# Optimization experiments

Measured on AMD Instinct MI355X. Metric: run time of the kernel, lower is better.

The kernel has to match this reference:

```python
import jax, jax.numpy as jnp
import numpy as np

B, T, D, H = 4, 2048, 1024, 16
HS = D // H  # 64
EPS = 1e-5


def layer_norm(x, g, b):
    mu = jnp.mean(x, axis=-1, keepdims=True)
    var = jnp.mean(jnp.square(x - mu), axis=-1, keepdims=True)
    return (x - mu) * jax.lax.rsqrt(var + EPS) * g + b


def setup_inputs() -> dict:
    key = jax.random.key(0)
    ks = jax.random.split(key, 12)
    s_in = 1.0 / np.sqrt(D)
    s_proj = 1.0 / np.sqrt(H * HS)
    s_ff = 1.0 / np.sqrt(4 * D)
    return {
        "x": jax.random.normal(ks[0], (B, T, D), jnp.float32),
        "ln1_g": jnp.ones((D,), jnp.float32),
        "ln1_b": jnp.zeros((D,), jnp.float32),
        # per-head Q/K/V weights stacked: [H, D, HS] (x @ W, no bias)
        "wq": jax.random.uniform(ks[1], (H, D, HS), jnp.float32, -s_in, s_in),
        "wk": jax.random.uniform(ks[2], (H, D, HS), jnp.float32, -s_in, s_in),
        "wv": jax.random.uniform(ks[3], (H, D, HS), jnp.float32, -s_in, s_in),
        "w_proj": jax.random.uniform(ks[4], (H * HS, D), jnp.float32, -s_proj, s_proj),
        "b_proj": jax.random.uniform(ks[5], (D,), jnp.float32, -s_proj, s_proj),
        "ln2_g": jnp.ones((D,), jnp.float32),
        "ln2_b": jnp.zeros((D,), jnp.float32),
        "w1": jax.random.uniform(ks[6], (D, 4 * D), jnp.float32, -s_in, s_in),
        "b1": jax.random.uniform(ks[7], (4 * D,), jnp.float32, -s_in, s_in),
        "w2": jax.random.uniform(ks[8], (4 * D, D), jnp.float32, -s_ff, s_ff),
        "b2": jax.random.uniform(ks[9], (D,), jnp.float32, -s_ff, s_ff),
    }


def reference(x, ln1_g, ln1_b, wq, wk, wv, w_proj, b_proj, ln2_g, ln2_b, w1, b1, w2, b2):
    # --- pre-LN self-attention ---
    xn = layer_norm(x, ln1_g, ln1_b)
    q = jnp.einsum("btd,hdk->bhtk", xn, wq)
    k = jnp.einsum("btd,hdk->bhtk", xn, wk)
    v = jnp.einsum("btd,hdk->bhtk", xn, wv)
    scale = HS ** -0.5
    scores = jnp.einsum("bhtk,bhsk->bhts", q, k) * scale  # [B,H,T,T]
    t = x.shape[1]
    causal = jnp.tril(jnp.ones((t, t), bool))
    scores = jnp.where(causal, scores, -jnp.inf)
    attn = jax.nn.softmax(scores, axis=-1)  # dropout p=0 -> identity
    ctx = jnp.einsum("bhts,bhsk->bhtk", attn, v)
    ctx = jnp.transpose(ctx, (0, 2, 1, 3)).reshape(x.shape[0], t, H * HS)
    x = x + ctx @ w_proj + b_proj
    # --- pre-LN feed-forward ---
    xn = layer_norm(x, ln2_g, ln2_b)
    h = jax.nn.relu(xn @ w1 + b1)
    return x + h @ w2 + b2
```

## Files before the change

### kernel.cpp

```cpp
#include <hip/hip_runtime.h>

typedef __bf16 bf16;
typedef __attribute__((ext_vector_type(8))) __bf16 bf16x8;
typedef __attribute__((ext_vector_type(4))) __bf16 bf16x4;
typedef __attribute__((ext_vector_type(4))) float f32x4;

static constexpr int Bc = 4, Tc = 2048, Dc = 1024, Hc = 16, HSc = 64, DFF = 4096;
static constexpr int Mrows = Bc * Tc;

#define DEV __device__ __forceinline__

DEV void load_lds16(const void* g, void* l) {
  __builtin_amdgcn_global_load_lds(
      (const __attribute__((address_space(1))) void*)g,
      (__attribute__((address_space(3))) void*)l, 16, 0, 0);
}

__global__ void repack_qkv_kernel(const float* __restrict__ wq,
                                  const float* __restrict__ wk,
                                  const float* __restrict__ wv,
                                  bf16* __restrict__ dst) {
  __shared__ float tile[64][65];
  const int dblk = blockIdx.x;
  const int z = blockIdx.y;
  const int w = z >> 4, h = z & 15;
  const float* src = (w == 0 ? wq : (w == 1 ? wk : wv)) + (size_t)h * Dc * HSc;
  const int tx = threadIdx.x, ty = threadIdx.y;
#pragma unroll
  for (int i = 0; i < 16; ++i)
    tile[ty + i * 4][tx] = src[(size_t)(dblk * 64 + ty + i * 4) * HSc + tx];
  __syncthreads();
#pragma unroll
  for (int i = 0; i < 16; ++i) {
    const int s = ty + i * 4;
    dst[((size_t)w * 1024 + h * 64 + s) * Dc + dblk * 64 + tx] = (bf16)tile[tx][s];
  }
}

__global__ void transpose_to_bf16_kernel(const float* __restrict__ src,
                                         bf16* __restrict__ dst, int R, int C) {
  __shared__ float tile[64][65];
  const int r0 = blockIdx.x * 64, c0 = blockIdx.y * 64;
  const int tx = threadIdx.x, ty = threadIdx.y;
#pragma unroll
  for (int i = 0; i < 16; ++i)
    tile[ty + i * 4][tx] = src[(size_t)(r0 + ty + i * 4) * C + c0 + tx];
  __syncthreads();
#pragma unroll
  for (int i = 0; i < 16; ++i)
    dst[(size_t)(c0 + ty + i * 4) * R + r0 + tx] = (bf16)tile[tx][ty + i * 4];
}

__global__ __launch_bounds__(256) void ln_kernel(const float* __restrict__ x,
                                                 const float* __restrict__ gam,
                                                 const float* __restrict__ bet,
                                                 bf16* __restrict__ out) {
  const int row = blockIdx.x;
  const int t = threadIdx.x;
  const float4 v = ((const float4*)(x + (size_t)row * Dc))[t];
  float s = v.x + v.y + v.z + v.w;
  float s2 = v.x * v.x + v.y * v.y + v.z * v.z + v.w * v.w;
#pragma unroll
  for (int m = 1; m < 64; m <<= 1) {
    s += __shfl_xor(s, m);
    s2 += __shfl_xor(s2, m);
  }
  __shared__ float red[8];
  const int wid = t >> 6;
  if ((t & 63) == 0) { red[wid * 2] = s; red[wid * 2 + 1] = s2; }
  __syncthreads();
  s = red[0] + red[2] + red[4] + red[6];
  s2 = red[1] + red[3] + red[5] + red[7];
  const float mean = s * (1.f / Dc);
  const float var = s2 * (1.f / Dc) - mean * mean;
  const float rstd = rsqrtf(var + 1e-5f);
  const float4 gv = ((const float4*)gam)[t];
  const float4 bv = ((const float4*)bet)[t];
  bf16x4 o;
  o[0] = (bf16)((v.x - mean) * rstd * gv.x + bv.x);
  o[1] = (bf16)((v.y - mean) * rstd * gv.y + bv.y);
  o[2] = (bf16)((v.z - mean) * rstd * gv.z + bv.z);
  o[3] = (bf16)((v.w - mean) * rstd * gv.w + bv.w);
  *(bf16x4*)(out + (size_t)row * Dc + t * 4) = o;
}

template <int MODE, int KTOT, int BN>
__global__ __launch_bounds__(512, 1) void gemm4p_kernel(
    const bf16* __restrict__ A, const bf16* __restrict__ BT,
    const float* __restrict__ bias, const float* __restrict__ resid,
    float* __restrict__ outf, bf16* __restrict__ outb,
    bf16* __restrict__ qo, bf16* __restrict__ ko, bf16* __restrict__ vto) {
  constexpr int NT = KTOT / 32;
  constexpr int L = (BN == 256) ? 4 : 3;
  constexpr int WN = (BN == 256) ? 4 : 2;
  constexpr int MW = (BN == 256) ? 128 : 64;
  constexpr int NAF = MW / 16;
  constexpr int NSTR = (MODE == 2) ? 4096 : 1024;
  constexpr int ABUF = 256 * 32 * 2;
  constexpr int BBUF = BN * 32 * 2;

  __shared__ __attribute__((aligned(16))) bf16 As[4][256 * 32];
  __shared__ __attribute__((aligned(16))) bf16 Bs[4][BN * 32];

  const int tid = threadIdx.x;
  const int wid = tid >> 6, lane = tid & 63;
  const int g = (lane >> 4) & 3, c = lane & 15;
  const int wm = wid / WN, wn = wid % WN;
  const int bm = blockIdx.x, bn = blockIdx.y;

  f32x4 acc[NAF][4];
#pragma unroll
  for (int i = 0; i < NAF; ++i)
#pragma unroll
    for (int j = 0; j < 4; ++j)
#pragma unroll
      for (int r = 0; r < 4; ++r) acc[i][j][r] = 0.f;

  const int sof = ((tid & 3) ^ ((tid >> 3) & 3)) << 4;
  const char* Agl = (const char*)A;
  const char* Bgl = (const char*)BT;

  auto stage = [&](int kt) {
    const int buf = kt & 3;
    const size_t kb = (size_t)kt * 64;
#pragma unroll
    for (int a = 0; a < 2; ++a)
      load_lds16(Agl + ((size_t)(bm * 256 + a * 128 + (tid >> 2)) * KTOT) * 2 + kb + sof,
                 (char*)&As[buf][0] + a * 8192 + tid * 16);
    if (BN == 256) {
#pragma unroll
      for (int a = 0; a < 2; ++a)
        load_lds16(Bgl + ((size_t)(bn * 256 + a * 128 + (tid >> 2)) * KTOT) * 2 + kb + sof,
                   (char*)&Bs[buf][0] + a * 8192 + tid * 16);
    } else {
      load_lds16(Bgl + ((size_t)(bn * 128 + (tid >> 2)) * KTOT) * 2 + kb + sof,
                 (char*)&Bs[buf][0] + tid * 16);
    }
  };

  stage(0);
  stage(1);
  stage(2);

  for (int t = 0; t < NT; ++t) {
    if (t + 2 < NT) {
      asm volatile("s_waitcnt vmcnt(%0)" ::"i"(2 * L) : "memory");
    } else if (t + 1 < NT) {
      asm volatile("s_waitcnt vmcnt(%0)" ::"i"(L) : "memory");
    } else {
      asm volatile("s_waitcnt vmcnt(0)" ::: "memory");
    }
    __builtin_amdgcn_s_barrier();
    if (t + 3 < NT) stage(t + 3);

    const char* Ab = (const char*)As + (t & 3) * ABUF;
    const char* Bb = (const char*)Bs + (t & 3) * BBUF;
    bf16x8 bfr[4], af[NAF];
#pragma unroll
    for (int j = 0; j < 4; ++j) {
      const int row = wn * 64 + j * 16 + c;
      bfr[j] = *(const bf16x8*)(Bb + row * 64 + ((g * 16) ^ (((row >> 1) & 3) << 4)));
    }
#pragma unroll
    for (int i = 0; i < NAF; ++i) {
      const int row = wm * MW + i * 16 + c;
      af[i] = *(const bf16x8*)(Ab + row * 64 + ((g * 16) ^ (((row >> 1) & 3) << 4)));
    }
    if (NAF == 8) {
      asm volatile("s_waitcnt lgkmcnt(4)" ::: "memory");
    } else {
      asm volatile("s_waitcnt lgkmcnt(0)" ::: "memory");
    }
    __builtin_amdgcn_sched_barrier(0);
    __builtin_amdgcn_s_setprio(1);
#pragma unroll
    for (int i = 0; i < 4; ++i)
#pragma unroll
      for (int j = 0; j < 4; ++j)
        acc[i][j] = __builtin_amdgcn_mfma_f32_16x16x32_bf16(af[i], bfr[j], acc[i][j], 0, 0, 0);
    __builtin_amdgcn_s_setprio(0);
    if (NAF == 8) {
      asm volatile("s_waitcnt lgkmcnt(0)" ::: "memory");
      __builtin_amdgcn_sched_barrier(0);
      __builtin_amdgcn_s_setprio(1);
#pragma unroll
      for (int i = 4; i < NAF; ++i)
#pragma unroll
        for (int j = 0; j < 4; ++j)
          acc[i][j] = __builtin_amdgcn_mfma_f32_16x16x32_bf16(af[i], bfr[j], acc[i][j], 0, 0, 0);
      __builtin_amdgcn_s_setprio(0);
    }
  }

#pragma unroll
  for (int nf = 0; nf < 4; ++nf) {
    const int n = bn * BN + wn * 64 + nf * 16 + c;
    float bi = 0.f;
    if (MODE != 0) bi = bias[n];
#pragma unroll
    for (int fr = 0; fr < NAF; ++fr) {
      const int m0 = bm * 256 + wm * MW + fr * 16 + g * 4;
      if (MODE == 0) {
        const int w = n >> 10, n1 = n & 1023, h = n1 >> 6, sidx = n1 & 63;
        const int b2 = m0 >> 11, t0 = m0 & 2047;
        if (w == 0) {
#pragma unroll
          for (int r = 0; r < 4; ++r)
            qo[(size_t)(b2 * Hc + h) * (Tc * HSc) + (size_t)(t0 + r) * HSc + sidx] =
                (bf16)(acc[fr][nf][r] * 0.125f);
        } else if (w == 1) {
#pragma unroll
          for (int r = 0; r < 4; ++r)
            ko[(size_t)(b2 * Hc + h) * (Tc * HSc) + (size_t)(t0 + r) * HSc + sidx] =
                (bf16)acc[fr][nf][r];
        } else {
          bf16x4 pk;
#pragma unroll
          for (int r = 0; r < 4; ++r) pk[r] = (bf16)acc[fr][nf][r];
          *(bf16x4*)&vto[((size_t)(b2 * Hc + h) * HSc + sidx) * Tc + t0] = pk;
        }
      } else if (MODE == 1 || MODE == 3) {
#pragma unroll
        for (int r = 0; r < 4; ++r) {
          const size_t idx = (size_t)(m0 + r) * NSTR + n;
          outf[idx] = acc[fr][nf][r] + bi + resid[idx];
        }
      } else {
#pragma unroll
        for (int r = 0; r < 4; ++r)
          outb[(size_t)(m0 + r) * NSTR + n] = (bf16)fmaxf(acc[fr][nf][r] + bi, 0.f);
      }
    }
  }
}

__global__ __launch_bounds__(256, 2) void attn_kernel(const bf16* __restrict__ q,
                                                      const bf16* __restrict__ k,
                                                      const bf16* __restrict__ vt,
                                                      bf16* __restrict__ ctx) {
  __shared__ __attribute__((aligned(16))) bf16 Kl[2][4096];
  __shared__ __attribute__((aligned(16))) bf16 Vl[2][4096];
  __shared__ __attribute__((aligned(16))) bf16 P[4][32][72];
  const int d0 = blockIdx.x;
  const int L = (d0 & 7) * 64 + (d0 >> 3);
  const int bh = L >> 3, p = L & 7;
  const int tid = threadIdx.x;
  const int wid = tid >> 6, lane = tid & 63;
  const int g = lane >> 4, c = lane & 15;
  const bf16* qh = q + (size_t)bh * Tc * HSc;
  const char* kh = (const char*)(k + (size_t)bh * Tc * HSc);
  const char* vh = (const char*)(vt + (size_t)bh * HSc * Tc);
  const int b = bh >> 4, h = bh & 15;

  const int sw = ((lane >> 3) & 7) << 4;
  const int soK = (lane * 16) ^ sw;
  const int vrow = lane >> 3;
  const int vcol = ((lane & 7) * 16) ^ sw;
  const int rsw = (c & 7) << 4;

  for (int g2 = 0; g2 < 2; ++g2) {
    const int grp = g2 ? p : 15 - p;
    const int ktB = 2 * grp + 1;
    const int ktW = 2 * grp + (wid >> 1);
    const int row0 = grp * 128 + wid * 32;
    const bf16* qb = qh + (size_t)row0 * HSc;

    bf16x8 qf[2][2];
#pragma unroll
    for (int mi = 0; mi < 2; ++mi)
#pragma unroll
      for (int kk = 0; kk < 2; ++kk)
        qf[mi][kk] = *(const bf16x8*)&qb[(size_t)(mi * 16 + c) * HSc + kk * 32 + g * 8];

    f32x4 o[2][4];
    float m_[2][4], ls[2][4];
#pragma unroll
    for (int mi = 0; mi < 2; ++mi)
#pragma unroll
      for (int r = 0; r < 4; ++r) {
        m_[mi][r] = -1e30f;
        ls[mi][r] = 0.f;
#pragma unroll
        for (int di = 0; di < 4; ++di) o[mi][di][r] = 0.f;
      }

    auto stage = [&](int buf, int kt) {
      const char* kb = kh + (size_t)kt * 8192;
      const char* vb = vh + (size_t)kt * 128;
#pragma unroll
      for (int i = 0; i < 4; ++i) {
        const int idx = wid * 4 + i;
        if (idx < 8) {
          load_lds16(kb + idx * 1024 + soK, (char*)&Kl[buf][0] + idx * 1024);
        } else {
          const int j = idx - 8;
          load_lds16(vb + (size_t)(j * 8 + vrow) * (Tc * 2) + vcol,
                     (char*)&Vl[buf][0] + j * 1024);
        }
      }
    };

    stage(0, 0);
    __syncthreads();
    int cur = 0;
    for (int kt = 0; kt <= ktB; ++kt) {
      if (kt < ktB) stage(cur ^ 1, kt + 1);
      if (kt <= ktW) {
        const char* Kb = (const char*)&Kl[cur][0];
        bf16x8 kf[4][2];
#pragma unroll
        for (int ni = 0; ni < 4; ++ni)
#pragma unroll
          for (int kk = 0; kk < 2; ++kk)
            kf[ni][kk] = *(const bf16x8*)(Kb + (ni * 16 + c) * 128 +
                                          (((kk << 6) | (g << 4)) ^ rsw));
        f32x4 s[2][4];
#pragma unroll
        for (int mi = 0; mi < 2; ++mi)
#pragma unroll
          for (int ni = 0; ni < 4; ++ni)
#pragma unroll
            for (int r = 0; r < 4; ++r) s[mi][ni][r] = 0.f;
        __builtin_amdgcn_s_setprio(1);
#pragma unroll
        for (int kk = 0; kk < 2; ++kk)
#pragma unroll
          for (int mi = 0; mi < 2; ++mi)
#pragma unroll
            for (int ni = 0; ni < 4; ++ni)
              s[mi][ni] = __builtin_amdgcn_mfma_f32_16x16x32_bf16(qf[mi][kk], kf[ni][kk],
                                                                  s[mi][ni], 0, 0, 0);
        __builtin_amdgcn_s_setprio(0);

        if (kt == ktW) {
#pragma unroll
          for (int mi = 0; mi < 2; ++mi)
#pragma unroll
            for (int ni = 0; ni < 4; ++ni)
#pragma unroll
              for (int r = 0; r < 4; ++r) {
                const int row = row0 + mi * 16 + g * 4 + r;
                const int col = kt * 64 + ni * 16 + c;
                if (col > row) s[mi][ni][r] = -1e30f;
              }
        }

        float pm[2][4];
        int need = 0;
#pragma unroll
        for (int mi = 0; mi < 2; ++mi)
#pragma unroll
          for (int r = 0; r < 4; ++r) {
            pm[mi][r] =
                fmaxf(fmaxf(s[mi][0][r], s[mi][1][r]), fmaxf(s[mi][2][r], s[mi][3][r]));
            need |= (pm[mi][r] > m_[mi][r] + 8.f) ? 1 : 0;
          }
        if (__any(need)) {
#pragma unroll
          for (int mi = 0; mi < 2; ++mi)
#pragma unroll
            for (int r = 0; r < 4; ++r) {
              float mx = pm[mi][r];
#pragma unroll
              for (int msk = 1; msk < 16; msk <<= 1) mx = fmaxf(mx, __shfl_xor(mx, msk));
              const float mn = fmaxf(m_[mi][r], mx);
              const float al = __expf(m_[mi][r] - mn);
              m_[mi][r] = mn;
              ls[mi][r] *= al;
#pragma unroll
              for (int di = 0; di < 4; ++di) o[mi][di][r] *= al;
            }
        }
#pragma unroll
        for (int mi = 0; mi < 2; ++mi)
#pragma unroll
          for (int r = 0; r < 4; ++r) {
            float ps = 0.f;
#pragma unroll
            for (int ni = 0; ni < 4; ++ni) {
              const float pv = __expf(s[mi][ni][r] - m_[mi][r]);
              ps += pv;
              P[wid][mi * 16 + g * 4 + r][ni * 16 + c] = (bf16)pv;
            }
            ls[mi][r] += ps;
          }
        asm volatile("s_waitcnt lgkmcnt(0)" ::: "memory");
        __builtin_amdgcn_sched_barrier(0);

        bf16x8 pf[2][2];
#pragma unroll
        for (int mi = 0; mi < 2; ++mi)
#pragma unroll
          for (int kk = 0; kk < 2; ++kk)
            pf[mi][kk] = *(const bf16x8*)&P[wid][mi * 16 + c][kk * 32 + g * 8];
        const char* Vb = (const char*)&Vl[cur][0];
#pragma unroll
        for (int di = 0; di < 4; ++di) {
          bf16x8 vf0 = *(const bf16x8*)(Vb + (di * 16 + c) * 128 + ((g << 4) ^ rsw));
          bf16x8 vf1 =
              *(const bf16x8*)(Vb + (di * 16 + c) * 128 + (((1 << 6) | (g << 4)) ^ rsw));
          __builtin_amdgcn_s_setprio(1);
#pragma unroll
          for (int mi = 0; mi < 2; ++mi) {
            o[mi][di] = __builtin_amdgcn_mfma_f32_16x16x32_bf16(pf[mi][0], vf0, o[mi][di], 0, 0, 0);
            o[mi][di] = __builtin_amdgcn_mfma_f32_16x16x32_bf16(pf[mi][1], vf1, o[mi][di], 0, 0, 0);
          }
          __builtin_amdgcn_s_setprio(0);
        }
      }
      __syncthreads();
      cur ^= 1;
    }

#pragma unroll
    for (int mi = 0; mi < 2; ++mi)
#pragma unroll
      for (int r = 0; r < 4; ++r) {
        float l = ls[mi][r];
#pragma unroll
        for (int msk = 1; msk < 16; msk <<= 1) l += __shfl_xor(l, msk);
        const float inv = 1.f / l;
        const int t = row0 + mi * 16 + g * 4 + r;
#pragma unroll
        for (int di = 0; di < 4; ++di)
          ctx[((size_t)(b * Tc + t)) * Dc + h * 64 + di * 16 + c] =
              (bf16)(o[mi][di][r] * inv);
      }
  }
}

extern "C" void kernel_launch(void* const* d_in, const int* in_sizes, int n_in,
                              void* d_out, int out_size, void* d_ws, size_t ws_size,
                              hipStream_t stream) {
  (void)in_sizes; (void)n_in; (void)out_size; (void)ws_size;
  const float* x      = (const float*)d_in[0];
  const float* ln1_g  = (const float*)d_in[1];
  const float* ln1_b  = (const float*)d_in[2];
  const float* wq     = (const float*)d_in[3];
  const float* wk     = (const float*)d_in[4];
  const float* wv     = (const float*)d_in[5];
  const float* w_proj = (const float*)d_in[6];
  const float* b_proj = (const float*)d_in[7];
  const float* ln2_g  = (const float*)d_in[8];
  const float* ln2_b  = (const float*)d_in[9];
  const float* w1     = (const float*)d_in[10];
  const float* b1     = (const float*)d_in[11];
  const float* w2     = (const float*)d_in[12];
  const float* b2     = (const float*)d_in[13];
  float* out = (float*)d_out;
  char* ws = (char*)d_ws;

  bf16* qbuf   = (bf16*)(ws + 0);
  bf16* kbuf   = (bf16*)(ws + 16777216);
  bf16* vtbuf  = (bf16*)(ws + 33554432);
  bf16* ctxbuf = (bf16*)(ws + 50331648);
  bf16* wqkvT  = (bf16*)(ws + 67108864);
  bf16* hbuf   = (bf16*)(ws + 0);
  bf16* wprojT = (bf16*)(ws + 73400320);
  bf16* w1T    = (bf16*)(ws + 75497472);
  bf16* w2T    = (bf16*)(ws + 83886080);
  bf16* xn     = (bf16*)(ws + 92274688);
  float* x1buf = (float*)(ws + 109051904);

  repack_qkv_kernel<<<dim3(16, 48), dim3(64, 4), 0, stream>>>(wq, wk, wv, wqkvT);
  transpose_to_bf16_kernel<<<dim3(16, 16), dim3(64, 4), 0, stream>>>(w_proj, wprojT, 1024, 1024);
  transpose_to_bf16_kernel<<<dim3(16, 64), dim3(64, 4), 0, stream>>>(w1, w1T, 1024, 4096);
  transpose_to_bf16_kernel<<<dim3(64, 16), dim3(64, 4), 0, stream>>>(w2, w2T, 4096, 1024);

  ln_kernel<<<Mrows, 256, 0, stream>>>(x, ln1_g, ln1_b, xn);
  gemm4p_kernel<0, 1024, 256><<<dim3(32, 12), 512, 0, stream>>>(
      xn, wqkvT, nullptr, nullptr, nullptr, nullptr, qbuf, kbuf, vtbuf);
  attn_kernel<<<512, 256, 0, stream>>>(qbuf, kbuf, vtbuf, ctxbuf);
  gemm4p_kernel<1, 1024, 128><<<dim3(32, 8), 512, 0, stream>>>(
      ctxbuf, wprojT, b_proj, x, x1buf, nullptr, nullptr, nullptr, nullptr);
  ln_kernel<<<Mrows, 256, 0, stream>>>(x1buf, ln2_g, ln2_b, xn);
  gemm4p_kernel<2, 1024, 256><<<dim3(32, 16), 512, 0, stream>>>(
      xn, w1T, b1, nullptr, nullptr, hbuf, nullptr, nullptr, nullptr);
  gemm4p_kernel<3, 4096, 128><<<dim3(32, 8), 512, 0, stream>>>(
      hbuf, w2T, b2, x1buf, out, nullptr, nullptr, nullptr, nullptr);
}
```

Baseline: 437.8 us.

## Restructure GEMM into 8-phase ping-pong pipeline with 64-wide K steps

Replaces the 4-buffer, 32-wide-K GEMM pipeline with a two-sided double buffer over 64-wide K tiles, split into two 32-wide halves. Global-to-LDS staging for future tiles is interleaved between MFMA phases, with barriers separating the phases, so memory traffic overlaps compute more finely. Warp tiling changes (4x2 warps for the BN=128 path), and the QKV projection now uses BN=128 tiles on a wider grid. The XOR swizzle on LDS reads is removed, which may introduce bank conflicts, and the extra barriers add synchronisation cost.

Result: faster. 385.1 us (-12.0%).

```diff
diff --git a/kernel.cpp b/kernel.cpp
--- a/kernel.cpp
+++ b/kernel.cpp
@@ -85,27 +85,26 @@
 }
 
 template <int MODE, int KTOT, int BN>
-__global__ __launch_bounds__(512, 1) void gemm4p_kernel(
+__global__ __launch_bounds__(512, 1) void gemm8p_kernel(
     const bf16* __restrict__ A, const bf16* __restrict__ BT,
     const float* __restrict__ bias, const float* __restrict__ resid,
     float* __restrict__ outf, bf16* __restrict__ outb,
     bf16* __restrict__ qo, bf16* __restrict__ ko, bf16* __restrict__ vto) {
-  constexpr int NT = KTOT / 32;
-  constexpr int L = (BN == 256) ? 4 : 3;
-  constexpr int WN = (BN == 256) ? 4 : 2;
-  constexpr int MW = (BN == 256) ? 128 : 64;
+  constexpr int NT = KTOT / 64;
+  constexpr int NSTR = (MODE == 2) ? 4096 : 1024;
+  constexpr int WMD = (BN == 256) ? 2 : 4;
+  constexpr int MW = 256 / WMD;
   constexpr int NAF = MW / 16;
-  constexpr int NSTR = (MODE == 2) ? 4096 : 1024;
-  constexpr int ABUF = 256 * 32 * 2;
-  constexpr int BBUF = BN * 32 * 2;
-
-  __shared__ __attribute__((aligned(16))) bf16 As[4][256 * 32];
-  __shared__ __attribute__((aligned(16))) bf16 Bs[4][BN * 32];
+  constexpr int NBI = BN / 128;
+
+  __shared__ __attribute__((aligned(16))) bf16 As[2][2][256 * 32];
+  __shared__ __attribute__((aligned(16))) bf16 Bs[2][2][BN * 32];
 
   const int tid = threadIdx.x;
   const int wid = tid >> 6, lane = tid & 63;
   const int g = (lane >> 4) & 3, c = lane & 15;
-  const int wm = wid / WN, wn = wid % WN;
+  const int wmi = (BN == 256) ? (wid >> 2) : (wid >> 1);
+  const int wni = (BN == 256) ? (wid & 3) : (wid & 1);
   const int bm = blockIdx.x, bn = blockIdx.y;
 
   f32x4 acc[NAF][4];
@@ -116,90 +115,165 @@
 #pragma unroll
       for (int r = 0; r < 4; ++r) acc[i][j][r] = 0.f;
 
-  const int sof = ((tid & 3) ^ ((tid >> 3) & 3)) << 4;
   const char* Agl = (const char*)A;
   const char* Bgl = (const char*)BT;
-
-  auto stage = [&](int kt) {
-    const int buf = kt & 3;
-    const size_t kb = (size_t)kt * 64;
+  const int grow = tid >> 2;
+  const int gcol = (tid & 3) * 8;
+
+  auto stageA = [&](int side, int ks, int kt) {
 #pragma unroll
     for (int a = 0; a < 2; ++a)
-      load_lds16(Agl + ((size_t)(bm * 256 + a * 128 + (tid >> 2)) * KTOT) * 2 + kb + sof,
-                 (char*)&As[buf][0] + a * 8192 + tid * 16);
+      load_lds16(
+          Agl + ((size_t)(bm * 256 + a * 128 + grow) * KTOT + kt * 64 + ks * 32 + gcol) * 2,
+          (char*)&As[side][ks][0] + a * 8192 + tid * 16);
+  };
+  auto stageB = [&](int side, int ks, int kt) {
+#pragma unroll
+    for (int b = 0; b < NBI; ++b)
+      load_lds16(
+          Bgl + ((size_t)(bn * BN + b * 128 + grow) * KTOT + kt * 64 + ks * 32 + gcol) * 2,
+          (char*)&Bs[side][ks][0] + b * 8192 + tid * 16);
+  };
+
+  const int aoff = (wmi * MW + c) * 64 + g * 16;
+  const int boff = (wni * 64 + c) * 64 + g * 16;
+
+  if (BN == 256) {
+    stageB(0, 0, 0); stageA(0, 0, 0); stageB(0, 1, 0); stageA(0, 1, 0);
+    stageB(1, 0, 1); stageA(1, 0, 1); stageB(1, 1, 1);
+    asm volatile("s_waitcnt vmcnt(6)" ::: "memory");
+  } else {
+    stageA(0, 0, 0); stageB(0, 0, 0); stageA(0, 1, 0); stageB(0, 1, 0);
+    stageA(1, 0, 1); stageB(1, 0, 1);
+    asm volatile("s_waitcnt vmcnt(3)" ::: "memory");
+  }
+  __builtin_amdgcn_s_barrier();
+
+  for (int t = 0; t < NT; ++t) {
+    const int s = t & 1, ns = s ^ 1;
+    const char* Ab0 = (const char*)&As[s][0][0] + aoff;
+    const char* Ab1 = (const char*)&As[s][1][0] + aoff;
+    const char* Bb0 = (const char*)&Bs[s][0][0] + boff;
+    const char* Bb1 = (const char*)&Bs[s][1][0] + boff;
+    bf16x8 af[4], bfr[4];
+
     if (BN == 256) {
 #pragma unroll
-      for (int a = 0; a < 2; ++a)
-        load_lds16(Bgl + ((size_t)(bn * 256 + a * 128 + (tid >> 2)) * KTOT) * 2 + kb + sof,
-                   (char*)&Bs[buf][0] + a * 8192 + tid * 16);
-    } else {
-      load_lds16(Bgl + ((size_t)(bn * 128 + (tid >> 2)) * KTOT) * 2 + kb + sof,
-                 (char*)&Bs[buf][0] + tid * 16);
-    }
-  };
-
-  stage(0);
-  stage(1);
-  stage(2);
-
-  for (int t = 0; t < NT; ++t) {
-    if (t + 2 < NT) {
-      asm volatile("s_waitcnt vmcnt(%0)" ::"i"(2 * L) : "memory");
-    } else if (t + 1 < NT) {
-      asm volatile("s_waitcnt vmcnt(%0)" ::"i"(L) : "memory");
-    } else {
-      asm volatile("s_waitcnt vmcnt(0)" ::: "memory");
-    }
-    __builtin_amdgcn_s_barrier();
-    if (t + 3 < NT) stage(t + 3);
-
-    const char* Ab = (const char*)As + (t & 3) * ABUF;
-    const char* Bb = (const char*)Bs + (t & 3) * BBUF;
-    bf16x8 bfr[4], af[NAF];
-#pragma unroll
-    for (int j = 0; j < 4; ++j) {
-      const int row = wn * 64 + j * 16 + c;
-      bfr[j] = *(const bf16x8*)(Bb + row * 64 + ((g * 16) ^ (((row >> 1) & 3) << 4)));
-    }
-#pragma unroll
-    for (int i = 0; i < NAF; ++i) {
-      const int row = wm * MW + i * 16 + c;
-      af[i] = *(const bf16x8*)(Ab + row * 64 + ((g * 16) ^ (((row >> 1) & 3) << 4)));
-    }
-    if (NAF == 8) {
-      asm volatile("s_waitcnt lgkmcnt(4)" ::: "memory");
-    } else {
-      asm volatile("s_waitcnt lgkmcnt(0)" ::: "memory");
-    }
-    __builtin_amdgcn_sched_barrier(0);
-    __builtin_amdgcn_s_setprio(1);
-#pragma unroll
-    for (int i = 0; i < 4; ++i)
-#pragma unroll
-      for (int j = 0; j < 4; ++j)
-        acc[i][j] = __builtin_amdgcn_mfma_f32_16x16x32_bf16(af[i], bfr[j], acc[i][j], 0, 0, 0);
-    __builtin_amdgcn_s_setprio(0);
-    if (NAF == 8) {
+      for (int f = 0; f < 4; ++f) af[f] = *(const bf16x8*)(Ab0 + f * 1024);
+#pragma unroll
+      for (int j = 0; j < 4; ++j) bfr[j] = *(const bf16x8*)(Bb0 + j * 1024);
+      if (t + 1 < NT) stageA(ns, 1, t + 1);
+      __builtin_amdgcn_s_barrier();
       asm volatile("s_waitcnt lgkmcnt(0)" ::: "memory");
       __builtin_amdgcn_sched_barrier(0);
       __builtin_amdgcn_s_setprio(1);
 #pragma unroll
-      for (int i = 4; i < NAF; ++i)
+      for (int f = 0; f < 4; ++f)
 #pragma unroll
         for (int j = 0; j < 4; ++j)
-          acc[i][j] = __builtin_amdgcn_mfma_f32_16x16x32_bf16(af[i], bfr[j], acc[i][j], 0, 0, 0);
+          acc[f][j] = __builtin_amdgcn_mfma_f32_16x16x32_bf16(af[f], bfr[j], acc[f][j], 0, 0, 0);
       __builtin_amdgcn_s_setprio(0);
+      __builtin_amdgcn_s_barrier();
+#pragma unroll
+      for (int f = 0; f < 4; ++f) af[f] = *(const bf16x8*)(Ab0 + (4 + f) * 1024);
+      if (t + 2 < NT) stageB(s, 0, t + 2);
+      __builtin_amdgcn_s_barrier();
+      asm volatile("s_waitcnt lgkmcnt(0)" ::: "memory");
+      __builtin_amdgcn_sched_barrier(0);
+      __builtin_amdgcn_s_setprio(1);
+#pragma unroll
+      for (int f = 0; f < 4; ++f)
+#pragma unroll
+        for (int j = 0; j < 4; ++j)
+          acc[4 + f][j] =
+              __builtin_amdgcn_mfma_f32_16x16x32_bf16(af[f], bfr[j], acc[4 + f][j], 0, 0, 0);
+      __builtin_amdgcn_s_setprio(0);
+      __builtin_amdgcn_s_barrier();
+#pragma unroll
+      for (int f = 0; f < 4; ++f) af[f] = *(const bf16x8*)(Ab1 + f * 1024);
+#pragma unroll
+      for (int j = 0; j < 4; ++j) bfr[j] = *(const bf16x8*)(Bb1 + j * 1024);
+      if (t + 2 < NT) stageA(s, 0, t + 2);
+      __builtin_amdgcn_s_barrier();
+      asm volatile("s_waitcnt lgkmcnt(0)" ::: "memory");
+      __builtin_amdgcn_sched_barrier(0);
+      __builtin_amdgcn_s_setprio(1);
+#pragma unroll
+      for (int f = 0; f < 4; ++f)
+#pragma unroll
+        for (int j = 0; j < 4; ++j)
+          acc[f][j] = __builtin_amdgcn_mfma_f32_16x16x32_bf16(af[f], bfr[j], acc[f][j], 0, 0, 0);
+      __builtin_amdgcn_s_setprio(0);
+      __builtin_amdgcn_s_barrier();
+#pragma unroll
+      for (int f = 0; f < 4; ++f) af[f] = *(const bf16x8*)(Ab1 + (4 + f) * 1024);
+      if (t + 2 < NT) stageB(s, 1, t + 2);
+      __builtin_amdgcn_s_barrier();
+      asm volatile("s_waitcnt lgkmcnt(0)" ::: "memory");
+      __builtin_amdgcn_sched_barrier(0);
+      __builtin_amdgcn_s_setprio(1);
+#pragma unroll
+      for (int f = 0; f < 4; ++f)
+#pragma unroll
+        for (int j = 0; j < 4; ++j)
+          acc[4 + f][j] =
+              __builtin_amdgcn_mfma_f32_16x16x32_bf16(af[f], bfr[j], acc[4 + f][j], 0, 0, 0);
+      __builtin_amdgcn_s_setprio(0);
+      if (t + 2 < NT) {
+        asm volatile("s_waitcnt vmcnt(6)" ::: "memory");
+      } else {
+        asm volatile("s_waitcnt vmcnt(0)" ::: "memory");
+      }
+      __builtin_amdgcn_s_barrier();
+    } else {
+#pragma unroll
+      for (int f = 0; f < 4; ++f) af[f] = *(const bf16x8*)(Ab0 + f * 1024);
+#pragma unroll
+      for (int j = 0; j < 4; ++j) bfr[j] = *(const bf16x8*)(Bb0 + j * 1024);
+      if (t + 1 < NT) { stageA(ns, 1, t + 1); stageB(ns, 1, t + 1); }
+      __builtin_amdgcn_s_barrier();
+      asm volatile("s_waitcnt lgkmcnt(0)" ::: "memory");
+      __builtin_amdgcn_sched_barrier(0);
+      __builtin_amdgcn_s_setprio(1);
+#pragma unroll
+      for (int f = 0; f < 4; ++f)
+#pragma unroll
+        for (int j = 0; j < 4; ++j)
+          acc[f][j] = __builtin_amdgcn_mfma_f32_16x16x32_bf16(af[f], bfr[j], acc[f][j], 0, 0, 0);
+      __builtin_amdgcn_s_setprio(0);
+      __builtin_amdgcn_s_barrier();
+#pragma unroll
+      for (int f = 0; f < 4; ++f) af[f] = *(const bf16x8*)(Ab1 + f * 1024);
+#pragma unroll
+      for (int j = 0; j < 4; ++j) bfr[j] = *(const bf16x8*)(Bb1 + j * 1024);
+      if (t + 2 < NT) { stageA(s, 0, t + 2); stageB(s, 0, t + 2); }
+      __builtin_amdgcn_s_barrier();
+      asm volatile("s_waitcnt lgkmcnt(0)" ::: "memory");
+      __builtin_amdgcn_sched_barrier(0);
+      __builtin_amdgcn_s_setprio(1);
+#pragma unroll
+      for (int f = 0; f < 4; ++f)
+#pragma unroll
+        for (int j = 0; j < 4; ++j)
+          acc[f][j] = __builtin_amdgcn_mfma_f32_16x16x32_bf16(af[f], bfr[j], acc[f][j], 0, 0, 0);
+      __builtin_amdgcn_s_setprio(0);
+      if (t + 2 < NT) {
+        asm volatile("s_waitcnt vmcnt(3)" ::: "memory");
+      } else {
+        asm volatile("s_waitcnt vmcnt(0)" ::: "memory");
+      }
+      __builtin_amdgcn_s_barrier();
     }
   }
 
 #pragma unroll
   for (int nf = 0; nf < 4; ++nf) {
-    const int n = bn * BN + wn * 64 + nf * 16 + c;
+    const int n = bn * BN + wni * 64 + nf * 16 + c;
     float bi = 0.f;
     if (MODE != 0) bi = bias[n];
 #pragma unroll
     for (int fr = 0; fr < NAF; ++fr) {
-      const int m0 = bm * 256 + wm * MW + fr * 16 + g * 4;
+      const int m0 = bm * 256 + wmi * MW + fr * 16 + g * 4;
       if (MODE == 0) {
         const int w = n >> 10, n1 = n & 1023, h = n1 >> 6, sidx = n1 & 63;
         const int b2 = m0 >> 11, t0 = m0 & 2047;
@@ -468,14 +542,14 @@
   transpose_to_bf16_kernel<<<dim3(64, 16), dim3(64, 4), 0, stream>>>(w2, w2T, 4096, 1024);
 
   ln_kernel<<<Mrows, 256, 0, stream>>>(x, ln1_g, ln1_b, xn);
-  gemm4p_kernel<0, 1024, 256><<<dim3(32, 12), 512, 0, stream>>>(
+  gemm8p_kernel<0, 1024, 128><<<dim3(32, 24), 512, 0, stream>>>(
       xn, wqkvT, nullptr, nullptr, nullptr, nullptr, qbuf, kbuf, vtbuf);
   attn_kernel<<<512, 256, 0, stream>>>(qbuf, kbuf, vtbuf, ctxbuf);
-  gemm4p_kernel<1, 1024, 128><<<dim3(32, 8), 512, 0, stream>>>(
+  gemm8p_kernel<1, 1024, 128><<<dim3(32, 8), 512, 0, stream>>>(
       ctxbuf, wprojT, b_proj, x, x1buf, nullptr, nullptr, nullptr, nullptr);
   ln_kernel<<<Mrows, 256, 0, stream>>>(x1buf, ln2_g, ln2_b, xn);
-  gemm4p_kernel<2, 1024, 256><<<dim3(32, 16), 512, 0, stream>>>(
+  gemm8p_kernel<2, 1024, 256><<<dim3(32, 16), 512, 0, stream>>>(
       xn, w1T, b1, nullptr, nullptr, hbuf, nullptr, nullptr, nullptr);
-  gemm4p_kernel<3, 4096, 128><<<dim3(32, 8), 512, 0, stream>>>(
+  gemm8p_kernel<3, 4096, 128><<<dim3(32, 8), 512, 0, stream>>>(
       hbuf, w2T, b2, x1buf, out, nullptr, nullptr, nullptr, nullptr);
 }
```

## Replace large 4-stage GEMM tiles with 128x128 double-buffered 256-thread kernel

Applied to the files above, without the earlier changes.

Replaces the 256xBN, 512-thread, 4-buffer GEMM with a 128x128 tile, 256-thread kernel that double-buffers through LDS and waits on a barrier before overwriting the active stage. The smaller tiles and lower LDS use allow several blocks per CU and give 2-4x more blocks in each grid, which aims to fix the low occupancy and wave-quantization of the old launches on the many-CU device. In exchange, each block reuses less data (more global/L2 traffic per FLOP), and the pipeline is shallower with an extra barrier per k-step.

Result: faster. 368.7 us (-15.8%).

```diff
diff --git a/kernel.cpp b/kernel.cpp
--- a/kernel.cpp
+++ b/kernel.cpp
@@ -84,122 +84,93 @@
   *(bf16x4*)(out + (size_t)row * Dc + t * 4) = o;
 }
 
-template <int MODE, int KTOT, int BN>
-__global__ __launch_bounds__(512, 1) void gemm4p_kernel(
+template <int MODE, int KTOT>
+__global__ __launch_bounds__(256) void gemmho_kernel(
     const bf16* __restrict__ A, const bf16* __restrict__ BT,
     const float* __restrict__ bias, const float* __restrict__ resid,
     float* __restrict__ outf, bf16* __restrict__ outb,
     bf16* __restrict__ qo, bf16* __restrict__ ko, bf16* __restrict__ vto) {
   constexpr int NT = KTOT / 32;
-  constexpr int L = (BN == 256) ? 4 : 3;
-  constexpr int WN = (BN == 256) ? 4 : 2;
-  constexpr int MW = (BN == 256) ? 128 : 64;
-  constexpr int NAF = MW / 16;
   constexpr int NSTR = (MODE == 2) ? 4096 : 1024;
-  constexpr int ABUF = 256 * 32 * 2;
-  constexpr int BBUF = BN * 32 * 2;
-
-  __shared__ __attribute__((aligned(16))) bf16 As[4][256 * 32];
-  __shared__ __attribute__((aligned(16))) bf16 Bs[4][BN * 32];
+
+  __shared__ __attribute__((aligned(16))) bf16 As[2][128 * 32];
+  __shared__ __attribute__((aligned(16))) bf16 Bs[2][128 * 32];
 
   const int tid = threadIdx.x;
   const int wid = tid >> 6, lane = tid & 63;
   const int g = (lane >> 4) & 3, c = lane & 15;
-  const int wm = wid / WN, wn = wid % WN;
+  const int wm = wid >> 1, wn = wid & 1;
   const int bm = blockIdx.x, bn = blockIdx.y;
 
-  f32x4 acc[NAF][4];
-#pragma unroll
-  for (int i = 0; i < NAF; ++i)
+  f32x4 acc[4][4];
+#pragma unroll
+  for (int i = 0; i < 4; ++i)
 #pragma unroll
     for (int j = 0; j < 4; ++j)
 #pragma unroll
       for (int r = 0; r < 4; ++r) acc[i][j][r] = 0.f;
 
-  const int sof = ((tid & 3) ^ ((tid >> 3) & 3)) << 4;
   const char* Agl = (const char*)A;
   const char* Bgl = (const char*)BT;
-
-  auto stage = [&](int kt) {
-    const int buf = kt & 3;
-    const size_t kb = (size_t)kt * 64;
+  const int grow = tid >> 2;
+  const int gsw = (((tid & 3) ^ ((tid >> 3) & 3)) << 4);
+
+  auto stage = [&](int side, int kt) {
 #pragma unroll
     for (int a = 0; a < 2; ++a)
-      load_lds16(Agl + ((size_t)(bm * 256 + a * 128 + (tid >> 2)) * KTOT) * 2 + kb + sof,
-                 (char*)&As[buf][0] + a * 8192 + tid * 16);
-    if (BN == 256) {
-#pragma unroll
-      for (int a = 0; a < 2; ++a)
-        load_lds16(Bgl + ((size_t)(bn * 256 + a * 128 + (tid >> 2)) * KTOT) * 2 + kb + sof,
-                   (char*)&Bs[buf][0] + a * 8192 + tid * 16);
-    } else {
-      load_lds16(Bgl + ((size_t)(bn * 128 + (tid >> 2)) * KTOT) * 2 + kb + sof,
-                 (char*)&Bs[buf][0] + tid * 16);
-    }
+      load_lds16(Agl + ((size_t)(bm * 128 + a * 64 + grow) * KTOT + kt * 32) * 2 + gsw,
+                 (char*)&As[side][0] + a * 4096 + tid * 16);
+#pragma unroll
+    for (int b = 0; b < 2; ++b)
+      load_lds16(Bgl + ((size_t)(bn * 128 + b * 64 + grow) * KTOT + kt * 32) * 2 + gsw,
+                 (char*)&Bs[side][0] + b * 4096 + tid * 16);
   };
 
-  stage(0);
-  stage(1);
-  stage(2);
+  const int rsw = ((c >> 1) & 3) << 4;
+  const int aoff = (wm * 64 + c) * 64 + ((g * 16) ^ rsw);
+  const int boff = (wn * 64 + c) * 64 + ((g * 16) ^ rsw);
+
+  stage(0, 0);
+  stage(1, 1);
+  asm volatile("s_waitcnt vmcnt(4)" ::: "memory");
+  __builtin_amdgcn_s_barrier();
 
   for (int t = 0; t < NT; ++t) {
+    const int s = t & 1;
+    const char* Ab = (const char*)&As[s][0] + aoff;
+    const char* Bb = (const char*)&Bs[s][0] + boff;
+    bf16x8 af[4], bfr[4];
+#pragma unroll
+    for (int f = 0; f < 4; ++f) af[f] = *(const bf16x8*)(Ab + f * 1024);
+#pragma unroll
+    for (int j = 0; j < 4; ++j) bfr[j] = *(const bf16x8*)(Bb + j * 1024);
+    asm volatile("s_waitcnt lgkmcnt(0)" ::: "memory");
+    __builtin_amdgcn_sched_barrier(0);
+    __builtin_amdgcn_s_barrier();
+    if (t + 2 < NT) stage(s, t + 2);
+    __builtin_amdgcn_s_setprio(1);
+#pragma unroll
+    for (int f = 0; f < 4; ++f)
+#pragma unroll
+      for (int j = 0; j < 4; ++j)
+        acc[f][j] = __builtin_amdgcn_mfma_f32_16x16x32_bf16(af[f], bfr[j], acc[f][j], 0, 0, 0);
+    __builtin_amdgcn_s_setprio(0);
     if (t + 2 < NT) {
-      asm volatile("s_waitcnt vmcnt(%0)" ::"i"(2 * L) : "memory");
-    } else if (t + 1 < NT) {
-      asm volatile("s_waitcnt vmcnt(%0)" ::"i"(L) : "memory");
+      asm volatile("s_waitcnt vmcnt(4)" ::: "memory");
     } else {
       asm volatile("s_waitcnt vmcnt(0)" ::: "memory");
     }
     __builtin_amdgcn_s_barrier();
-    if (t + 3 < NT) stage(t + 3);
-
-    const char* Ab = (const char*)As + (t & 3) * ABUF;
-    const char* Bb = (const char*)Bs + (t & 3) * BBUF;
-    bf16x8 bfr[4], af[NAF];
-#pragma unroll
-    for (int j = 0; j < 4; ++j) {
-      const int row = wn * 64 + j * 16 + c;
-      bfr[j] = *(const bf16x8*)(Bb + row * 64 + ((g * 16) ^ (((row >> 1) & 3) << 4)));
-    }
-#pragma unroll
-    for (int i = 0; i < NAF; ++i) {
-      const int row = wm * MW + i * 16 + c;
-      af[i] = *(const bf16x8*)(Ab + row * 64 + ((g * 16) ^ (((row >> 1) & 3) << 4)));
-    }
-    if (NAF == 8) {
-      asm volatile("s_waitcnt lgkmcnt(4)" ::: "memory");
-    } else {
-      asm volatile("s_waitcnt lgkmcnt(0)" ::: "memory");
-    }
-    __builtin_amdgcn_sched_barrier(0);
-    __builtin_amdgcn_s_setprio(1);
-#pragma unroll
-    for (int i = 0; i < 4; ++i)
-#pragma unroll
-      for (int j = 0; j < 4; ++j)
-        acc[i][j] = __builtin_amdgcn_mfma_f32_16x16x32_bf16(af[i], bfr[j], acc[i][j], 0, 0, 0);
-    __builtin_amdgcn_s_setprio(0);
-    if (NAF == 8) {
-      asm volatile("s_waitcnt lgkmcnt(0)" ::: "memory");
-      __builtin_amdgcn_sched_barrier(0);
-      __builtin_amdgcn_s_setprio(1);
-#pragma unroll
-      for (int i = 4; i < NAF; ++i)
-#pragma unroll
-        for (int j = 0; j < 4; ++j)
-          acc[i][j] = __builtin_amdgcn_mfma_f32_16x16x32_bf16(af[i], bfr[j], acc[i][j], 0, 0, 0);
-      __builtin_amdgcn_s_setprio(0);
-    }
   }
 
 #pragma unroll
   for (int nf = 0; nf < 4; ++nf) {
-    const int n = bn * BN + wn * 64 + nf * 16 + c;
+    const int n = bn * 128 + wn * 64 + nf * 16 + c;
     float bi = 0.f;
     if (MODE != 0) bi = bias[n];
 #pragma unroll
-    for (int fr = 0; fr < NAF; ++fr) {
-      const int m0 = bm * 256 + wm * MW + fr * 16 + g * 4;
+    for (int fr = 0; fr < 4; ++fr) {
+      const int m0 = bm * 128 + wm * 64 + fr * 16 + g * 4;
       if (MODE == 0) {
         const int w = n >> 10, n1 = n & 1023, h = n1 >> 6, sidx = n1 & 63;
         const int b2 = m0 >> 11, t0 = m0 & 2047;
@@ -468,14 +439,14 @@
   transpose_to_bf16_kernel<<<dim3(64, 16), dim3(64, 4), 0, stream>>>(w2, w2T, 4096, 1024);
 
   ln_kernel<<<Mrows, 256, 0, stream>>>(x, ln1_g, ln1_b, xn);
-  gemm4p_kernel<0, 1024, 256><<<dim3(32, 12), 512, 0, stream>>>(
+  gemmho_kernel<0, 1024><<<dim3(64, 24), 256, 0, stream>>>(
       xn, wqkvT, nullptr, nullptr, nullptr, nullptr, qbuf, kbuf, vtbuf);
   attn_kernel<<<512, 256, 0, stream>>>(qbuf, kbuf, vtbuf, ctxbuf);
-  gemm4p_kernel<1, 1024, 128><<<dim3(32, 8), 512, 0, stream>>>(
+  gemmho_kernel<1, 1024><<<dim3(64, 8), 256, 0, stream>>>(
       ctxbuf, wprojT, b_proj, x, x1buf, nullptr, nullptr, nullptr, nullptr);
   ln_kernel<<<Mrows, 256, 0, stream>>>(x1buf, ln2_g, ln2_b, xn);
-  gemm4p_kernel<2, 1024, 256><<<dim3(32, 16), 512, 0, stream>>>(
+  gemmho_kernel<2, 1024><<<dim3(64, 32), 256, 0, stream>>>(
       xn, w1T, b1, nullptr, nullptr, hbuf, nullptr, nullptr, nullptr);
-  gemm4p_kernel<3, 4096, 128><<<dim3(32, 8), 512, 0, stream>>>(
+  gemmho_kernel<3, 4096><<<dim3(64, 8), 256, 0, stream>>>(
       hbuf, w2T, b2, x1buf, out, nullptr, nullptr, nullptr, nullptr);
 }
```
